# Performance work log

Hardware: AMD Instinct MI355X
Metric: run time of the kernel (lower is better)

The kernel has to match this reference:

```python
import jax, jax.numpy as jnp
import numpy as np

B, C_IN, T = 64, 9, 4096
HIDDEN, OUT = 128, 10
NEW_T = T // 4            # two MaxPool1d(2) stages
N_NODES = B * NEW_T       # 65536 flattened nodes
N_EDGES = 524288


def setup_inputs() -> dict:
    key = jax.random.key(0)
    ks = jax.random.split(key, 8)
    def w(k, sh, fan):
        return jax.random.normal(k, sh, jnp.float32) * (1.0 / np.sqrt(fan))
    return {
        "x": jax.random.normal(ks[0], (B, C_IN, T), jnp.float32),
        "edge_index": jax.random.randint(ks[1], (2, N_EDGES), 0, N_NODES, dtype=jnp.int32),
        "conv1_w": w(ks[2], (16, C_IN, 5), C_IN * 5),
        "conv1_b": jnp.zeros((16,), jnp.float32),
        "conv2_w": w(ks[3], (32, 16, 5), 16 * 5),
        "conv2_b": jnp.zeros((32,), jnp.float32),
        "gcn1_w": w(ks[4], (32, HIDDEN), 32),
        "gcn1_b": jnp.zeros((HIDDEN,), jnp.float32),
        "gcn2_w": w(ks[5], (HIDDEN, HIDDEN), HIDDEN),
        "gcn2_b": jnp.zeros((HIDDEN,), jnp.float32),
        "cls_w": w(ks[6], (HIDDEN, OUT), HIDDEN),
        "cls_b": jnp.zeros((OUT,), jnp.float32),
    }


def _conv1d(x, w, b):
    # x: [B, C, T], w: [O, I, K], 'same' padding (pad=2, k=5)
    y = jax.lax.conv_general_dilated(x, w, (1,), [(2, 2)],
                                     dimension_numbers=("NCH", "OIH", "NCH"))
    return y + b[None, :, None]


def _maxpool2(x):
    return jax.lax.reduce_window(x, -jnp.inf, jax.lax.max, (1, 1, 2), (1, 1, 2), "VALID")


def _gcn(x, w, b, src, dst):
    # PyG GCNConv: add self-loops, symmetric D^{-1/2}(A+I)D^{-1/2} X W + b
    h = x @ w
    deg = jnp.zeros((N_NODES,), x.dtype).at[dst].add(1.0) + 1.0  # +1 for self-loop
    dinv = jax.lax.rsqrt(deg)
    coef = dinv[src] * dinv[dst]                      # [E]
    agg = jnp.zeros_like(h).at[dst].add(h[src] * coef[:, None])
    agg = agg + h * (dinv * dinv)[:, None]            # self-loop contribution
    return agg + b


def reference(x, edge_index, conv1_w, conv1_b, conv2_w, conv2_b,
              gcn1_w, gcn1_b, gcn2_w, gcn2_b, cls_w, cls_b):
    h = _maxpool2(jax.nn.relu(_conv1d(x, conv1_w, conv1_b)))   # [B,16,T/2]
    h = _maxpool2(jax.nn.relu(_conv1d(h, conv2_w, conv2_b)))   # [B,32,T/4]
    feats = h.transpose(0, 2, 1).reshape(-1, 32)               # [B*NEW_T, 32]
    src, dst = edge_index[0], edge_index[1]
    g = jax.nn.relu(_gcn(feats, gcn1_w, gcn1_b, src, dst))
    g = jax.nn.relu(_gcn(g, gcn2_w, gcn2_b, src, dst))
    pooled = g.reshape(B, NEW_T, HIDDEN).mean(axis=1)          # mean over nodes per graph
    return pooled @ cls_w + cls_b                              # [B, OUT]
```

## Files before the change

kernel.cpp:

```cpp
#include <hip/hip_runtime.h>
#include <hip/hip_bf16.h>

typedef __hip_bfloat16 bf16;
typedef unsigned short ushort8_v __attribute__((ext_vector_type(8)));
typedef short bf16x8 __attribute__((ext_vector_type(8)));
typedef float f32x4 __attribute__((ext_vector_type(4)));

#define N_B     64
#define C_IN    9
#define T0      4096
#define C1      16
#define T1      2048
#define C2      32
#define T2      1024
#define N_NODES 65536
#define N_EDGES 524288
#define HID     128
#define OUT_C   10
#define SLOT_CAP 32

__device__ __forceinline__ float us2f(unsigned short u) {
  union { unsigned int i; float f; } c; c.i = ((unsigned int)u) << 16; return c.f;
}
__device__ __forceinline__ unsigned short f2us(float f) {
  bf16 h = __float2bfloat16(f);
  unsigned short u;
  __builtin_memcpy(&u, &h, 2);
  return u;
}


__global__ __launch_bounds__(256) void init_kernel(int* __restrict__ cnt, float* __restrict__ pooled)
{
  int i = blockIdx.x * 256 + threadIdx.x;
  if (i < N_NODES) cnt[i] = 0;
  if (i < N_B * HID) pooled[i] = 0.f;
}

__global__ __launch_bounds__(256) void conv1_scatter_kernel(const float* __restrict__ x, const float* __restrict__ w1,
                                                            const float* __restrict__ b1,
                                                            const int* __restrict__ ei, int* __restrict__ cnt,
                                                            unsigned short* __restrict__ slots,
                                                            unsigned short* __restrict__ y1)
{
  __shared__ float sx[C_IN * 136];
  __shared__ float sw[45 * 17];
  __shared__ float sb[C1];
  int tid = threadIdx.x;
  if (blockIdx.x < 2048) {
    int e = blockIdx.x * 256 + tid;
    int d = ei[N_EDGES + e];
    int s = ei[e];
    int r = atomicAdd(&cnt[d], 1);
    if (r < SLOT_CAP) slots[((size_t)d << 5) + r] = (unsigned short)s;
    return;
  }
  int blk = blockIdx.x - 2048;
  int b = blk >> 5;
  int P0 = (blk & 31) << 6;
  int t0 = 2 * P0 - 2;
  for (int i = tid; i < C_IN * 132; i += 256) {
    int c = i / 132, j = i % 132;
    int t = t0 + j;
    sx[c * 136 + j] = (t >= 0 && t < T0) ? x[(size_t)(b * C_IN + c) * T0 + t] : 0.f;
  }
  for (int i = tid; i < C1 * 45; i += 256) sw[(i % 45) * 17 + i / 45] = w1[i];
  if (tid < C1) sb[tid] = b1[tid];
  __syncthreads();

  int o = tid & 15, pg = tid >> 4;
  float bias = sb[o];
  float a[8];
  #pragma unroll
  for (int i = 0; i < 8; ++i) a[i] = bias;
  #pragma unroll
  for (int c = 0; c < C_IN; ++c) {
    float xv[12];
    #pragma unroll
    for (int q = 0; q < 3; ++q)
      *(float4*)&xv[4 * q] = *(const float4*)&sx[c * 136 + 8 * pg + 4 * q];
    const float* wr = &sw[(c * 5) * 17 + o];
    float w0 = wr[0], w1_ = wr[17], w2_ = wr[34], w3_ = wr[51], w4_ = wr[68];
    #pragma unroll
    for (int m = 0; m < 8; ++m)
      a[m] += xv[m]*w0 + xv[m+1]*w1_ + xv[m+2]*w2_ + xv[m+3]*w3_ + xv[m+4]*w4_;
  }
  ushort4 r;
  r.x = f2us(fmaxf(fmaxf(a[0], a[1]), 0.f));
  r.y = f2us(fmaxf(fmaxf(a[2], a[3]), 0.f));
  r.z = f2us(fmaxf(fmaxf(a[4], a[5]), 0.f));
  r.w = f2us(fmaxf(fmaxf(a[6], a[7]), 0.f));
  *(ushort4*)&y1[(size_t)(b * C1 + o) * T1 + P0 + 4 * pg] = r;
}

__global__ __launch_bounds__(256) void dinv_kernel(const int* __restrict__ cnt, float* __restrict__ dinv)
{
  int i = blockIdx.x * 256 + threadIdx.x;
  if (i < N_NODES) dinv[i] = rsqrtf((float)cnt[i] + 1.0f);
}

__global__ __launch_bounds__(256) void conv2_kernel(const unsigned short* __restrict__ y1, const float* __restrict__ w2,
                                                    const float* __restrict__ b2, const float* __restrict__ dinv,
                                                    unsigned short* __restrict__ feats)
{
  __shared__ float sy[C1 * 72];
  __shared__ float sw[80 * 33];
  __shared__ float sb[C2];
  int tid = threadIdx.x;
  int b = blockIdx.x >> 5;
  int Q0 = (blockIdx.x & 31) << 5;
  int t0 = 2 * Q0 - 2;
  for (int i = tid; i < C1 * 68; i += 256) {
    int c = i / 68, j = i % 68;
    int t = t0 + j;
    sy[c * 72 + j] = (t >= 0 && t < T1) ? us2f(y1[(size_t)(b * C1 + c) * T1 + t]) : 0.f;
  }
  for (int i = tid; i < C2 * 80; i += 256) sw[(i % 80) * 33 + i / 80] = w2[i];
  if (tid < C2) sb[tid] = b2[tid];
  __syncthreads();

  int o = tid & 31, pg = tid >> 5;
  float bias = sb[o];
  float a[8];
  #pragma unroll
  for (int i = 0; i < 8; ++i) a[i] = bias;
  #pragma unroll
  for (int c = 0; c < C1; ++c) {
    float yv[12];
    #pragma unroll
    for (int q = 0; q < 3; ++q)
      *(float4*)&yv[4 * q] = *(const float4*)&sy[c * 72 + 8 * pg + 4 * q];
    const float* wr = &sw[(c * 5) * 33 + o];
    float w0 = wr[0], w1_ = wr[33], w2_ = wr[66], w3_ = wr[99], w4_ = wr[132];
    #pragma unroll
    for (int m = 0; m < 8; ++m)
      a[m] += yv[m]*w0 + yv[m+1]*w1_ + yv[m+2]*w2_ + yv[m+3]*w3_ + yv[m+4]*w4_;
  }
  #pragma unroll
  for (int i = 0; i < 4; ++i) {
    int node = (b << 10) + Q0 + 4 * pg + i;
    float dv = dinv[node];
    feats[(size_t)node * C2 + o] = f2us(fmaxf(fmaxf(a[2*i], a[2*i+1]), 0.f) * dv);
  }
}

__global__ __launch_bounds__(256) void aggX_kernel(const unsigned short* __restrict__ F, const int* __restrict__ cnt,
                                                   const unsigned short* __restrict__ slots,
                                                   const float* __restrict__ dinv,
                                                   unsigned short* __restrict__ aggXb)
{
  int tid = threadIdx.x;
  int node = (blockIdx.x << 6) + (tid >> 2);
  int jq = (tid & 3) << 3;
  float dn = dinv[node];
  float acc[8];
  {
    ushort8_v r = *(const ushort8_v*)(F + (size_t)node * C2 + jq);
    #pragma unroll
    for (int k = 0; k < 8; ++k) acc[k] = us2f(r[k]);
  }
  const unsigned short* sl = slots + ((size_t)node << 5);
  int e1 = min(cnt[node], SLOT_CAP);
  int e = 0;
  for (; e + 2 <= e1; e += 2) {
    int s0 = sl[e], s1 = sl[e + 1];
    ushort8_v r0 = *(const ushort8_v*)(F + (size_t)s0 * C2 + jq);
    ushort8_v r1 = *(const ushort8_v*)(F + (size_t)s1 * C2 + jq);
    #pragma unroll
    for (int k = 0; k < 8; ++k) acc[k] += us2f(r0[k]) + us2f(r1[k]);
  }
  if (e < e1) {
    int s0 = sl[e];
    ushort8_v r0 = *(const ushort8_v*)(F + (size_t)s0 * C2 + jq);
    #pragma unroll
    for (int k = 0; k < 8; ++k) acc[k] += us2f(r0[k]);
  }
  ushort8_v o;
  #pragma unroll
  for (int k = 0; k < 8; ++k) o[k] = f2us(acc[k] * dn);
  *(ushort8_v*)(aggXb + (size_t)node * C2 + jq) = o;
}

__global__ __launch_bounds__(256) void gemm12_kernel(const unsigned short* __restrict__ aggXb,
                                                     const float* __restrict__ W1, const float* __restrict__ gb1,
                                                     const float* __restrict__ W2, const float* __restrict__ dinv,
                                                     unsigned short* __restrict__ Hb)
{
  __shared__ unsigned short sw1[32 * 36 * 4];
  __shared__ unsigned short sG[64 * 132];
  __shared__ unsigned short sw2[HID * 132];
  int tid = threadIdx.x;
  int n0b = blockIdx.x << 6;

  for (int i = tid; i < 32 * 32; i += 256) {
    int k = i >> 5, j4 = (i & 31) << 2;
    float4 v = *(const float4*)&W1[(size_t)k * HID + j4];
    sw1[(j4 + 0) * 36 + k] = f2us(v.x);
    sw1[(j4 + 1) * 36 + k] = f2us(v.y);
    sw1[(j4 + 2) * 36 + k] = f2us(v.z);
    sw1[(j4 + 3) * 36 + k] = f2us(v.w);
  }
  for (int i = tid; i < HID * 32; i += 256) {
    int k = i >> 5, j4 = (i & 31) << 2;
    float4 v = *(const float4*)&W2[(size_t)k * HID + j4];
    sw2[(j4 + 0) * 132 + k] = f2us(v.x);
    sw2[(j4 + 1) * 132 + k] = f2us(v.y);
    sw2[(j4 + 2) * 132 + k] = f2us(v.z);
    sw2[(j4 + 3) * 132 + k] = f2us(v.w);
  }
  __syncthreads();

  int w = tid >> 6, l = tid & 63;
  int lr = l & 15, lk = l >> 4;
  int nloc = w << 4;

  bf16x8 af1 = *(const bf16x8*)((const short*)aggXb + (size_t)(n0b + nloc + lr) * C2 + lk * 8);
  #pragma unroll
  for (int jt = 0; jt < 8; ++jt) {
    f32x4 acc = {0.f, 0.f, 0.f, 0.f};
    bf16x8 bf = *(const bf16x8*)((const short*)sw1 + (size_t)(jt * 16 + lr) * 36 + lk * 8);
    acc = __builtin_amdgcn_mfma_f32_16x16x32_bf16(af1, bf, acc, 0, 0, 0);
    float bj = gb1[jt * 16 + lr];
    #pragma unroll
    for (int r = 0; r < 4; ++r)
      sG[(size_t)(nloc + lk * 4 + r) * 132 + jt * 16 + lr] = f2us(fmaxf(acc[r] + bj, 0.f));
  }
  __syncthreads();

  bf16x8 af2[4];
  #pragma unroll
  for (int ks = 0; ks < 4; ++ks)
    af2[ks] = *(const bf16x8*)((const short*)sG + (size_t)(nloc + lr) * 132 + ks * 32 + lk * 8);
  float4 dv = *(const float4*)&dinv[n0b + nloc + lk * 4];
  float dvr[4] = {dv.x, dv.y, dv.z, dv.w};
  #pragma unroll
  for (int nt = 0; nt < 8; ++nt) {
    f32x4 acc = {0.f, 0.f, 0.f, 0.f};
    #pragma unroll
    for (int ks = 0; ks < 4; ++ks) {
      bf16x8 bf = *(const bf16x8*)((const short*)sw2 + (size_t)(nt * 16 + lr) * 132 + ks * 32 + lk * 8);
      acc = __builtin_amdgcn_mfma_f32_16x16x32_bf16(af2[ks], bf, acc, 0, 0, 0);
    }
    #pragma unroll
    for (int r = 0; r < 4; ++r)
      Hb[(size_t)(n0b + nloc + lk * 4 + r) * HID + nt * 16 + lr] = f2us(acc[r] * dvr[r]);
  }
}

__global__ __launch_bounds__(256) void agg2_pool_kernel(const unsigned short* __restrict__ Hb, const int* __restrict__ cnt,
                                                        const unsigned short* __restrict__ slots,
                                                        const float* __restrict__ dinv,
                                                        const float* __restrict__ bias, float* __restrict__ pooled)
{
  __shared__ float red[16][HID];
  int tid = threadIdx.x;
  int g = tid >> 4;
  int jq = (tid & 15) << 3;
  int node = (blockIdx.x << 4) + g;
  float dn = dinv[node];
  float acc[8];
  {
    ushort8_v r = *(const ushort8_v*)(Hb + (size_t)node * HID + jq);
    #pragma unroll
    for (int k = 0; k < 8; ++k) acc[k] = us2f(r[k]);
  }
  const unsigned short* sl = slots + ((size_t)node << 5);
  int e1 = min(cnt[node], SLOT_CAP);
  int e = 0;
  for (; e + 2 <= e1; e += 2) {
    int s0 = sl[e], s1 = sl[e + 1];
    ushort8_v r0 = *(const ushort8_v*)(Hb + (size_t)s0 * HID + jq);
    ushort8_v r1 = *(const ushort8_v*)(Hb + (size_t)s1 * HID + jq);
    #pragma unroll
    for (int k = 0; k < 8; ++k) acc[k] += us2f(r0[k]) + us2f(r1[k]);
  }
  if (e < e1) {
    int s0 = sl[e];
    ushort8_v r0 = *(const ushort8_v*)(Hb + (size_t)s0 * HID + jq);
    #pragma unroll
    for (int k = 0; k < 8; ++k) acc[k] += us2f(r0[k]);
  }
  #pragma unroll
  for (int k = 0; k < 8; ++k)
    red[g][jq + k] = fmaxf(dn * acc[k] + bias[jq + k], 0.f);
  __syncthreads();
  if (tid < HID) {
    float s = 0.f;
    #pragma unroll
    for (int g2 = 0; g2 < 16; ++g2) s += red[g2][tid];
    int b = blockIdx.x >> 6;
    atomicAdd(&pooled[b * HID + tid], s * (1.0f / 1024.0f));
  }
}


__global__ __launch_bounds__(64) void cls_kernel(const float* __restrict__ pooled, const float* __restrict__ w,
                                                 const float* __restrict__ cb, float* __restrict__ out)
{
  int b = blockIdx.x, o = threadIdx.x;
  if (o < OUT_C) {
    float acc = cb[o];
    for (int i = 0; i < HID; ++i)
      acc += pooled[b * HID + i] * w[i * OUT_C + o];
    out[b * OUT_C + o] = acc;
  }
}


extern "C" void kernel_launch(void* const* d_in, const int* in_sizes, int n_in,
                              void* d_out, int out_size, void* d_ws, size_t ws_size,
                              hipStream_t stream)
{
  const float* x    = (const float*)d_in[0];
  const int*   ei   = (const int*)d_in[1];
  const float* c1w  = (const float*)d_in[2];
  const float* c1b  = (const float*)d_in[3];
  const float* c2w  = (const float*)d_in[4];
  const float* c2b  = (const float*)d_in[5];
  const float* g1w  = (const float*)d_in[6];
  const float* g1b  = (const float*)d_in[7];
  const float* g2w  = (const float*)d_in[8];
  const float* g2b  = (const float*)d_in[9];
  const float* clsw = (const float*)d_in[10];
  const float* clsb = (const float*)d_in[11];
  float* outp = (float*)d_out;

  char* ws = (char*)d_ws;
  size_t off_b = 0;
  auto alloc = [&](size_t bytes) { void* p = ws + off_b; off_b = (off_b + bytes + 255) & ~(size_t)255; return p; };
  int*   cnt    = (int*)  alloc((size_t)N_NODES * 4);
  float* dinvv  = (float*)alloc((size_t)N_NODES * 4);
  unsigned short* slots = (unsigned short*)alloc((size_t)N_NODES * SLOT_CAP * 2);
  unsigned short* y1    = (unsigned short*)alloc((size_t)N_B * C1 * T1 * 2);
  unsigned short* feats = (unsigned short*)alloc((size_t)N_NODES * C2 * 2);
  unsigned short* aggXb = (unsigned short*)alloc((size_t)N_NODES * C2 * 2);
  unsigned short* H     = (unsigned short*)alloc((size_t)N_NODES * HID * 2);
  float* pooled = (float*)alloc((size_t)N_B * HID * 4);
  (void)ws_size; (void)in_sizes; (void)n_in; (void)out_size;

  init_kernel         <<<256, 256, 0, stream>>>(cnt, pooled);
  conv1_scatter_kernel<<<4096, 256, 0, stream>>>(x, c1w, c1b, ei, cnt, slots, y1);
  dinv_kernel         <<<N_NODES / 256, 256, 0, stream>>>(cnt, dinvv);

  conv2_kernel<<<2048, 256, 0, stream>>>(y1, c2w, c2b, dinvv, feats);

  aggX_kernel<<<N_NODES / 64, 256, 0, stream>>>(feats, cnt, slots, dinvv, aggXb);

  gemm12_kernel<<<N_NODES / 64, 256, 0, stream>>>(aggXb, g1w, g1b, g2w, dinvv, H);

  agg2_pool_kernel<<<N_NODES / 16, 256, 0, stream>>>(H, cnt, slots, dinvv, g2b, pooled);

  cls_kernel<<<N_B, 64, 0, stream>>>(pooled, clsw, clsb, outp);
}
```

Before: 119.6 us.

## Drop dinv kernel, pretranspose GCN weights once, restructure gemm12 to read weights globally

```diff
diff --git a/kernel.cpp b/kernel.cpp
--- a/kernel.cpp
+++ b/kernel.cpp
@@ -30,11 +30,22 @@
 }
 
 
-__global__ __launch_bounds__(256) void init_kernel(int* __restrict__ cnt, float* __restrict__ pooled)
-{
-  int i = blockIdx.x * 256 + threadIdx.x;
-  if (i < N_NODES) cnt[i] = 0;
-  if (i < N_B * HID) pooled[i] = 0.f;
+__global__ __launch_bounds__(256) void init_kernel(int* __restrict__ cnt, float* __restrict__ pooled,
+                                                   const float* __restrict__ W1, const float* __restrict__ W2,
+                                                   unsigned short* __restrict__ W1T, unsigned short* __restrict__ W2T)
+{
+  int gid = blockIdx.x * 256 + threadIdx.x;
+  if (gid < N_NODES) cnt[gid] = 0;
+  if (gid < N_B * HID) pooled[gid] = 0.f;
+  if (gid < HID * HID) {
+    int j = gid >> 7, k = gid & 127;
+    W2T[j * HID + k] = f2us(W2[(size_t)k * HID + j]);
+  }
+  if (gid >= 32768 && gid < 32768 + HID * 32) {
+    int i = gid - 32768;
+    int j = i >> 5, k = i & 31;
+    W1T[j * 32 + k] = f2us(W1[(size_t)k * HID + j]);
+  }
 }
 
 __global__ __launch_bounds__(256) void conv1_scatter_kernel(const float* __restrict__ x, const float* __restrict__ w1,
@@ -93,14 +104,8 @@
   *(ushort4*)&y1[(size_t)(b * C1 + o) * T1 + P0 + 4 * pg] = r;
 }
 
-__global__ __launch_bounds__(256) void dinv_kernel(const int* __restrict__ cnt, float* __restrict__ dinv)
-{
-  int i = blockIdx.x * 256 + threadIdx.x;
-  if (i < N_NODES) dinv[i] = rsqrtf((float)cnt[i] + 1.0f);
-}
-
 __global__ __launch_bounds__(256) void conv2_kernel(const unsigned short* __restrict__ y1, const float* __restrict__ w2,
-                                                    const float* __restrict__ b2, const float* __restrict__ dinv,
+                                                    const float* __restrict__ b2, const int* __restrict__ cnt,
                                                     unsigned short* __restrict__ feats)
 {
   __shared__ float sy[C1 * 72];
@@ -139,20 +144,20 @@
   #pragma unroll
   for (int i = 0; i < 4; ++i) {
     int node = (b << 10) + Q0 + 4 * pg + i;
-    float dv = dinv[node];
+    float dv = rsqrtf((float)cnt[node] + 1.0f);
     feats[(size_t)node * C2 + o] = f2us(fmaxf(fmaxf(a[2*i], a[2*i+1]), 0.f) * dv);
   }
 }
 
 __global__ __launch_bounds__(256) void aggX_kernel(const unsigned short* __restrict__ F, const int* __restrict__ cnt,
                                                    const unsigned short* __restrict__ slots,
-                                                   const float* __restrict__ dinv,
                                                    unsigned short* __restrict__ aggXb)
 {
   int tid = threadIdx.x;
   int node = (blockIdx.x << 6) + (tid >> 2);
   int jq = (tid & 3) << 3;
-  float dn = dinv[node];
+  int cn = cnt[node];
+  float dn = rsqrtf((float)cn + 1.0f);
   float acc[8];
   {
     ushort8_v r = *(const ushort8_v*)(F + (size_t)node * C2 + jq);
@@ -160,7 +165,7 @@
     for (int k = 0; k < 8; ++k) acc[k] = us2f(r[k]);
   }
   const unsigned short* sl = slots + ((size_t)node << 5);
-  int e1 = min(cnt[node], SLOT_CAP);
+  int e1 = min(cn, SLOT_CAP);
   int e = 0;
   for (; e + 2 <= e1; e += 2) {
     int s0 = sl[e], s1 = sl[e + 1];
@@ -182,74 +187,68 @@
 }
 
 __global__ __launch_bounds__(256) void gemm12_kernel(const unsigned short* __restrict__ aggXb,
-                                                     const float* __restrict__ W1, const float* __restrict__ gb1,
-                                                     const float* __restrict__ W2, const float* __restrict__ dinv,
+                                                     const unsigned short* __restrict__ W1T,
+                                                     const float* __restrict__ gb1,
+                                                     const unsigned short* __restrict__ W2T,
+                                                     const int* __restrict__ cnt,
                                                      unsigned short* __restrict__ Hb)
 {
-  __shared__ unsigned short sw1[32 * 36 * 4];
   __shared__ unsigned short sG[64 * 132];
-  __shared__ unsigned short sw2[HID * 132];
-  int tid = threadIdx.x;
-  int n0b = blockIdx.x << 6;
-
-  for (int i = tid; i < 32 * 32; i += 256) {
-    int k = i >> 5, j4 = (i & 31) << 2;
-    float4 v = *(const float4*)&W1[(size_t)k * HID + j4];
-    sw1[(j4 + 0) * 36 + k] = f2us(v.x);
-    sw1[(j4 + 1) * 36 + k] = f2us(v.y);
-    sw1[(j4 + 2) * 36 + k] = f2us(v.z);
-    sw1[(j4 + 3) * 36 + k] = f2us(v.w);
-  }
-  for (int i = tid; i < HID * 32; i += 256) {
-    int k = i >> 5, j4 = (i & 31) << 2;
-    float4 v = *(const float4*)&W2[(size_t)k * HID + j4];
-    sw2[(j4 + 0) * 132 + k] = f2us(v.x);
-    sw2[(j4 + 1) * 132 + k] = f2us(v.y);
-    sw2[(j4 + 2) * 132 + k] = f2us(v.z);
-    sw2[(j4 + 3) * 132 + k] = f2us(v.w);
-  }
-  __syncthreads();
-
+  int tid = threadIdx.x;
   int w = tid >> 6, l = tid & 63;
   int lr = l & 15, lk = l >> 4;
-  int nloc = w << 4;
-
-  bf16x8 af1 = *(const bf16x8*)((const short*)aggXb + (size_t)(n0b + nloc + lr) * C2 + lk * 8);
-  #pragma unroll
-  for (int jt = 0; jt < 8; ++jt) {
-    f32x4 acc = {0.f, 0.f, 0.f, 0.f};
-    bf16x8 bf = *(const bf16x8*)((const short*)sw1 + (size_t)(jt * 16 + lr) * 36 + lk * 8);
-    acc = __builtin_amdgcn_mfma_f32_16x16x32_bf16(af1, bf, acc, 0, 0, 0);
-    float bj = gb1[jt * 16 + lr];
-    #pragma unroll
-    for (int r = 0; r < 4; ++r)
-      sG[(size_t)(nloc + lk * 4 + r) * 132 + jt * 16 + lr] = f2us(fmaxf(acc[r] + bj, 0.f));
+  int n0b = blockIdx.x << 6;
+
+  {
+    int nb = w << 4;
+    bf16x8 af = *(const bf16x8*)((const short*)aggXb + (size_t)(n0b + nb + lr) * C2 + lk * 8);
+    #pragma unroll
+    for (int jt = 0; jt < 8; ++jt) {
+      bf16x8 bfr = *(const bf16x8*)((const short*)W1T + (jt * 16 + lr) * 32 + lk * 8);
+      f32x4 acc = {0.f, 0.f, 0.f, 0.f};
+      acc = __builtin_amdgcn_mfma_f32_16x16x32_bf16(af, bfr, acc, 0, 0, 0);
+      float bj = gb1[jt * 16 + lr];
+      #pragma unroll
+      for (int r = 0; r < 4; ++r)
+        sG[(nb + lk * 4 + r) * 132 + jt * 16 + lr] = f2us(fmaxf(acc[r] + bj, 0.f));
+    }
   }
   __syncthreads();
 
-  bf16x8 af2[4];
-  #pragma unroll
-  for (int ks = 0; ks < 4; ++ks)
-    af2[ks] = *(const bf16x8*)((const short*)sG + (size_t)(nloc + lr) * 132 + ks * 32 + lk * 8);
-  float4 dv = *(const float4*)&dinv[n0b + nloc + lk * 4];
-  float dvr[4] = {dv.x, dv.y, dv.z, dv.w};
-  #pragma unroll
-  for (int nt = 0; nt < 8; ++nt) {
-    f32x4 acc = {0.f, 0.f, 0.f, 0.f};
-    #pragma unroll
-    for (int ks = 0; ks < 4; ++ks) {
-      bf16x8 bf = *(const bf16x8*)((const short*)sw2 + (size_t)(nt * 16 + lr) * 132 + ks * 32 + lk * 8);
-      acc = __builtin_amdgcn_mfma_f32_16x16x32_bf16(af2[ks], bf, acc, 0, 0, 0);
+  {
+    int jb = w << 5;
+    bf16x8 bfr[2][4];
+    #pragma unroll
+    for (int jtt = 0; jtt < 2; ++jtt)
+      #pragma unroll
+      for (int ks = 0; ks < 4; ++ks)
+        bfr[jtt][ks] = *(const bf16x8*)((const short*)W2T + (size_t)(jb + jtt * 16 + lr) * HID + ks * 32 + lk * 8);
+    #pragma unroll
+    for (int nt = 0; nt < 4; ++nt) {
+      bf16x8 afr[4];
+      #pragma unroll
+      for (int ks = 0; ks < 4; ++ks)
+        afr[ks] = *(const bf16x8*)((const short*)sG + (nt * 16 + lr) * 132 + ks * 32 + lk * 8);
+      int rowb = n0b + nt * 16 + lk * 4;
+      int4 c4 = *(const int4*)&cnt[rowb];
+      float dvr[4] = { rsqrtf((float)c4.x + 1.f), rsqrtf((float)c4.y + 1.f),
+                       rsqrtf((float)c4.z + 1.f), rsqrtf((float)c4.w + 1.f) };
+      #pragma unroll
+      for (int jtt = 0; jtt < 2; ++jtt) {
+        f32x4 acc = {0.f, 0.f, 0.f, 0.f};
+        #pragma unroll
+        for (int ks = 0; ks < 4; ++ks)
+          acc = __builtin_amdgcn_mfma_f32_16x16x32_bf16(afr[ks], bfr[jtt][ks], acc, 0, 0, 0);
+        #pragma unroll
+        for (int r = 0; r < 4; ++r)
+          Hb[(size_t)(rowb + r) * HID + jb + jtt * 16 + lr] = f2us(acc[r] * dvr[r]);
+      }
     }
-    #pragma unroll
-    for (int r = 0; r < 4; ++r)
-      Hb[(size_t)(n0b + nloc + lk * 4 + r) * HID + nt * 16 + lr] = f2us(acc[r] * dvr[r]);
   }
 }
 
 __global__ __launch_bounds__(256) void agg2_pool_kernel(const unsigned short* __restrict__ Hb, const int* __restrict__ cnt,
                                                         const unsigned short* __restrict__ slots,
-                                                        const float* __restrict__ dinv,
                                                         const float* __restrict__ bias, float* __restrict__ pooled)
 {
   __shared__ float red[16][HID];
@@ -257,7 +256,8 @@
   int g = tid >> 4;
   int jq = (tid & 15) << 3;
   int node = (blockIdx.x << 4) + g;
-  float dn = dinv[node];
+  int cn = cnt[node];
+  float dn = rsqrtf((float)cn + 1.0f);
   float acc[8];
   {
     ushort8_v r = *(const ushort8_v*)(Hb + (size_t)node * HID + jq);
@@ -265,7 +265,7 @@
     for (int k = 0; k < 8; ++k) acc[k] = us2f(r[k]);
   }
   const unsigned short* sl = slots + ((size_t)node << 5);
-  int e1 = min(cnt[node], SLOT_CAP);
+  int e1 = min(cn, SLOT_CAP);
   int e = 0;
   for (; e + 2 <= e1; e += 2) {
     int s0 = sl[e], s1 = sl[e + 1];
@@ -329,8 +329,9 @@
   size_t off_b = 0;
   auto alloc = [&](size_t bytes) { void* p = ws + off_b; off_b = (off_b + bytes + 255) & ~(size_t)255; return p; };
   int*   cnt    = (int*)  alloc((size_t)N_NODES * 4);
-  float* dinvv  = (float*)alloc((size_t)N_NODES * 4);
   unsigned short* slots = (unsigned short*)alloc((size_t)N_NODES * SLOT_CAP * 2);
+  unsigned short* w1t   = (unsigned short*)alloc((size_t)HID * 32 * 2);
+  unsigned short* w2t   = (unsigned short*)alloc((size_t)HID * HID * 2);
   unsigned short* y1    = (unsigned short*)alloc((size_t)N_B * C1 * T1 * 2);
   unsigned short* feats = (unsigned short*)alloc((size_t)N_NODES * C2 * 2);
   unsigned short* aggXb = (unsigned short*)alloc((size_t)N_NODES * C2 * 2);
@@ -338,17 +339,16 @@
   float* pooled = (float*)alloc((size_t)N_B * HID * 4);
   (void)ws_size; (void)in_sizes; (void)n_in; (void)out_size;
 
-  init_kernel         <<<256, 256, 0, stream>>>(cnt, pooled);
+  init_kernel         <<<256, 256, 0, stream>>>(cnt, pooled, g1w, g2w, w1t, w2t);
   conv1_scatter_kernel<<<4096, 256, 0, stream>>>(x, c1w, c1b, ei, cnt, slots, y1);
-  dinv_kernel         <<<N_NODES / 256, 256, 0, stream>>>(cnt, dinvv);
-
-  conv2_kernel<<<2048, 256, 0, stream>>>(y1, c2w, c2b, dinvv, feats);
-
-  aggX_kernel<<<N_NODES / 64, 256, 0, stream>>>(feats, cnt, slots, dinvv, aggXb);
-
-  gemm12_kernel<<<N_NODES / 64, 256, 0, stream>>>(aggXb, g1w, g1b, g2w, dinvv, H);
-
-  agg2_pool_kernel<<<N_NODES / 16, 256, 0, stream>>>(H, cnt, slots, dinvv, g2b, pooled);
+
+  conv2_kernel<<<2048, 256, 0, stream>>>(y1, c2w, c2b, cnt, feats);
+
+  aggX_kernel<<<N_NODES / 64, 256, 0, stream>>>(feats, cnt, slots, aggXb);
+
+  gemm12_kernel<<<N_NODES / 64, 256, 0, stream>>>(aggXb, w1t, g1b, w2t, cnt, H);
+
+  agg2_pool_kernel<<<N_NODES / 16, 256, 0, stream>>>(H, cnt, slots, g2b, pooled);
 
   cls_kernel<<<N_B, 64, 0, stream>>>(pooled, clsw, clsb, outp);
 }
```

New measurement: 110.8 us. 7.3% less time.
